# Kernel optimization log

Hardware: AMD Instinct MI355X
Metric: run time of the kernel (lower is better)

## Reference

```python
import jax, jax.numpy as jnp
import numpy as np
import math

N_EMBD = 768
N_HEAD = 12
D_HEAD = N_EMBD // N_HEAD  # 64, used ONLY for the score scale (matches the torch code)
B, S = 4, 2048


def setup_inputs() -> dict:
    key = jax.random.key(0)
    ks = jax.random.split(key, 9)
    scale = 1.0 / math.sqrt(N_EMBD)
    return {
        "x": jax.random.normal(ks[0], (B, S, N_EMBD), dtype=jnp.float32),
        # per-head full-width projections, stacked over heads: [H, E, E]
        "Wq": jax.random.normal(ks[1], (N_HEAD, N_EMBD, N_EMBD), dtype=jnp.float32) * scale,
        "Wk": jax.random.normal(ks[2], (N_HEAD, N_EMBD, N_EMBD), dtype=jnp.float32) * scale,
        "Wv": jax.random.normal(ks[3], (N_HEAD, N_EMBD, N_EMBD), dtype=jnp.float32) * scale,
        "bq": jax.random.normal(ks[4], (N_HEAD, N_EMBD), dtype=jnp.float32) * scale,
        "bk": jax.random.normal(ks[5], (N_HEAD, N_EMBD), dtype=jnp.float32) * scale,
        "bv": jax.random.normal(ks[6], (N_HEAD, N_EMBD), dtype=jnp.float32) * scale,
        # output projection: [H*E, E]
        "W0": jax.random.normal(ks[7], (N_HEAD * N_EMBD, N_EMBD), dtype=jnp.float32) * (1.0 / math.sqrt(N_HEAD * N_EMBD)),
        "b0": jax.random.normal(ks[8], (N_EMBD,), dtype=jnp.float32) * scale,
    }


def reference(x, Wq, Wk, Wv, bq, bk, bv, W0, b0):
    # Per-head projections, vectorized over heads: [B, H, S, E]
    q = jnp.einsum("bse,hef->bhsf", x, Wq) + bq[None, :, None, :]
    k = jnp.einsum("bse,hef->bhsf", x, Wk) + bk[None, :, None, :]
    v = jnp.einsum("bse,hef->bhsf", x, Wv) + bv[None, :, None, :]
    # scores: q @ k^T / sqrt(d_head)  (note: scale uses d_head, NOT n_embd, per source)
    scores = jnp.einsum("bhse,bhte->bhst", q, k) / math.sqrt(D_HEAD)
    attn = jax.nn.softmax(scores, axis=-1)  # no causal mask in the source
    y = jnp.einsum("bhst,bhte->bhse", attn, v)  # [B, H, S, E]
    # concat heads along feature dim in head order: [B, S, H*E]
    z = jnp.transpose(y, (0, 2, 1, 3)).reshape(B, S, N_HEAD * N_EMBD)
    return z @ W0 + b0
```

## Files before the change

### kernel.cpp

```cpp
#include <hip/hip_runtime.h>
#include <cstdint>
#include <cstddef>


#define DEV __device__ __forceinline__

using bf16x8 = __attribute__((ext_vector_type(8))) short;
using f32x4  = __attribute__((ext_vector_type(4))) float;
using su8    = __attribute__((ext_vector_type(8))) unsigned short;

DEV unsigned short f2b(float x) {
  unsigned u = __builtin_bit_cast(unsigned, x);
  u += 0x7fffu + ((u >> 16) & 1u);
  return (unsigned short)(u >> 16);
}

DEV void gld_lds16(const void* g, void* l) {
  __builtin_amdgcn_global_load_lds(
      (const __attribute__((address_space(1))) void*)g,
      (__attribute__((address_space(3))) void*)l,
      16, 0, 0);
}

template <int EPI>
__global__ __launch_bounds__(256)
void gemm_bt_k(const unsigned short* __restrict__ A, long az, int lda,
               const unsigned short* __restrict__ Bt, long bz, int ldb,
               void* __restrict__ C, long cz, int ldc,
               int K, float scale, const float* __restrict__ bias, int biasz)
{
  __shared__ unsigned short lsA[128 * 32];
  __shared__ unsigned short lsB[128 * 32];

  const int tid  = threadIdx.x;
  const int lane = tid & 63;
  const int wid  = tid >> 6;
  const int wr   = wid >> 1, wc = wid & 1;
  const int z    = blockIdx.z;
  const int m0   = blockIdx.x * 128;
  const int n0   = blockIdx.y * 128;

  A  += (size_t)z * az;
  Bt += (size_t)z * bz;

  f32x4 acc[4][4];
#pragma unroll
  for (int i = 0; i < 4; i++)
#pragma unroll
    for (int j = 0; j < 4; j++) acc[i][j] = (f32x4){0.f, 0.f, 0.f, 0.f};

  const int srow = lane >> 2;
  const int scol = (lane & 3) * 8;
  const int fr   = lane & 15;
  const int kq   = lane >> 4;

  for (int k0 = 0; k0 < K; k0 += 32) {
    __syncthreads();
#pragma unroll
    for (int i = 0; i < 2; i++) {
      int c = wid * 2 + i;
      int r = c * 16 + srow;
      gld_lds16(A  + (size_t)(m0 + r) * lda + (k0 + scol), &lsA[c * 512]);
      gld_lds16(Bt + (size_t)(n0 + r) * ldb + (k0 + scol), &lsB[c * 512]);
    }
    __syncthreads();

    bf16x8 af[4], bfr[4];
#pragma unroll
    for (int mi = 0; mi < 4; mi++)
      af[mi] = *(const bf16x8*)&lsA[(wr * 64 + mi * 16 + fr) * 32 + kq * 8];
#pragma unroll
    for (int ni = 0; ni < 4; ni++)
      bfr[ni] = *(const bf16x8*)&lsB[(wc * 64 + ni * 16 + fr) * 32 + kq * 8];
#pragma unroll
    for (int mi = 0; mi < 4; mi++)
#pragma unroll
      for (int ni = 0; ni < 4; ni++)
        acc[mi][ni] = __builtin_amdgcn_mfma_f32_16x16x32_bf16(af[mi], bfr[ni], acc[mi][ni], 0, 0, 0);
  }

  const int rb = m0 + wr * 64 + (lane >> 4) * 4;
  const int cb = n0 + wc * 64 + (lane & 15);

  if (EPI == 0) {
    unsigned short* Co = (unsigned short*)C + (size_t)z * cz;
#pragma unroll
    for (int mi = 0; mi < 4; mi++)
#pragma unroll
      for (int ni = 0; ni < 4; ni++) {
        int col = cb + ni * 16;
        float badd = bias ? bias[(size_t)z * biasz + col] : 0.f;
#pragma unroll
        for (int r = 0; r < 4; r++) {
          float v = acc[mi][ni][r] * scale + badd;
          Co[(size_t)(rb + mi * 16 + r) * ldc + col] = f2b(v);
        }
      }
  } else if (EPI == 1) {
    float* Co = (float*)C + (size_t)z * cz;
#pragma unroll
    for (int mi = 0; mi < 4; mi++)
#pragma unroll
      for (int ni = 0; ni < 4; ni++) {
        int col = cb + ni * 16;
#pragma unroll
        for (int r = 0; r < 4; r++)
          atomicAdd(&Co[(size_t)(rb + mi * 16 + r) * ldc + col], acc[mi][ni][r]);
      }
  } else {
    float* Co = (float*)C + (size_t)z * cz;
#pragma unroll
    for (int mi = 0; mi < 4; mi++)
#pragma unroll
      for (int ni = 0; ni < 4; ni++) {
        int col = cb + ni * 16;
#pragma unroll
        for (int r = 0; r < 4; r++)
          Co[(size_t)(rb + mi * 16 + r) * ldc + col] = acc[mi][ni][r] * scale;
      }
  }
}

__global__ __launch_bounds__(256)
void cast_k(const float* __restrict__ s, unsigned short* __restrict__ d, long n4)
{
  long i = (long)blockIdx.x * 256 + threadIdx.x;
  long stride = (long)gridDim.x * 256;
  for (; i < n4; i += stride) {
    float4 v = ((const float4*)s)[i];
    ushort4 o = { f2b(v.x), f2b(v.y), f2b(v.z), f2b(v.w) };
    ((ushort4*)d)[i] = o;
  }
}

__global__ __launch_bounds__(256)
void tcast_k(const float* __restrict__ src, unsigned short* __restrict__ dst)
{
  __shared__ unsigned short t[64][65];
  const int R = 768;
  const int r0 = blockIdx.x * 64, c0 = blockIdx.y * 64;
  const float* s = src + (size_t)blockIdx.z * R * R;
  unsigned short* d = dst + (size_t)blockIdx.z * R * R;
  const int tx = threadIdx.x & 63, ty = threadIdx.x >> 6;
#pragma unroll
  for (int i = 0; i < 16; i++) {
    int r = ty * 16 + i;
    t[r][tx] = f2b(s[(size_t)(r0 + r) * R + c0 + tx]);
  }
  __syncthreads();
#pragma unroll
  for (int i = 0; i < 16; i++) {
    int r = ty * 16 + i;
    d[(size_t)(c0 + r) * R + r0 + tx] = t[tx][r];
  }
}

__global__ __launch_bounds__(256)
void obias1_k(const float* __restrict__ pbv, const float* __restrict__ pW0,
              float* __restrict__ obp)
{
  int f = blockIdx.x * 256 + threadIdx.x;
  int c = blockIdx.y;
  int g0 = c * 256;
  float a = 0.f;
#pragma unroll 4
  for (int g = g0; g < g0 + 256; ++g) a += pbv[g] * pW0[(size_t)g * 768 + f];
  obp[(size_t)c * 768 + f] = a;
}

__global__ __launch_bounds__(256)
void obias2_k(const float* __restrict__ pb0, const float* __restrict__ obp,
              float* __restrict__ ob)
{
  int f = blockIdx.x * 256 + threadIdx.x;
  float a = pb0[f];
#pragma unroll
  for (int c = 0; c < 36; ++c) a += obp[(size_t)c * 768 + f];
  ob[f] = a;
}

__global__ __launch_bounds__(256)
void init_out_k(float4* __restrict__ out, const float4* __restrict__ ob, long n4)
{
  long i = (long)blockIdx.x * 256 + threadIdx.x;
  long stride = (long)gridDim.x * 256;
  for (; i < n4; i += stride) out[i] = ob[i % 192];
}

__global__ __launch_bounds__(256)
void softmax_rows_k(float* __restrict__ Sb)
{
  const int t = threadIdx.x;
  float* rowf = Sb + ((size_t)blockIdx.y * 2048 + blockIdx.x) * 2048;
  float4 a = ((const float4*)rowf)[t * 2];
  float4 b = ((const float4*)rowf)[t * 2 + 1];
  float v[8] = {a.x, a.y, a.z, a.w, b.x, b.y, b.z, b.w};

  float m = v[0];
#pragma unroll
  for (int j = 1; j < 8; j++) m = fmaxf(m, v[j]);
#pragma unroll
  for (int o = 1; o < 64; o <<= 1) m = fmaxf(m, __shfl_xor(m, o));
  __shared__ float red[8];
  if ((t & 63) == 0) red[t >> 6] = m;
  __syncthreads();
  m = fmaxf(fmaxf(red[0], red[1]), fmaxf(red[2], red[3]));

  float e[8], s = 0.f;
#pragma unroll
  for (int j = 0; j < 8; j++) { e[j] = __expf(v[j] - m); s += e[j]; }
#pragma unroll
  for (int o = 1; o < 64; o <<= 1) s += __shfl_xor(s, o);
  if ((t & 63) == 0) red[4 + (t >> 6)] = s;
  __syncthreads();
  s = red[4] + red[5] + red[6] + red[7];
  float rs = 1.f / s;

  unsigned short* rowb = (unsigned short*)rowf;
  su8 o8;
#pragma unroll
  for (int j = 0; j < 8; j++) o8[j] = f2b(e[j] * rs);
  *(su8*)&rowb[t * 8] = o8;
}

extern "C" void kernel_launch(void* const* d_in, const int* in_sizes, int n_in,
                              void* d_out, int out_size, void* d_ws, size_t ws_size,
                              hipStream_t stream)
{
  const long E = 768, S = 2048, H = 12, NB = 4;
  const long EE = E * E;
  const long SE = S * E;
  const long SS = S * S;

  const float* x   = (const float*)d_in[0];
  const float* Wq  = (const float*)d_in[1];
  const float* Wk  = (const float*)d_in[2];
  const float* Wv  = (const float*)d_in[3];
  const float* bq  = (const float*)d_in[4];
  const float* bk  = (const float*)d_in[5];
  const float* bv  = (const float*)d_in[6];
  const float* W0  = (const float*)d_in[7];
  const float* pb0 = (const float*)d_in[8];
  float* out = (float*)d_out;

  char* w = (char*)d_ws;
  size_t off = 0;
  auto take = [&](size_t bytes) -> char* {
    char* p = w + off;
    off += (bytes + 255) & ~(size_t)255;
    return p;
  };
  unsigned short* xb    = (unsigned short*)take(NB * SE * 2);
  unsigned short* WqTb  = (unsigned short*)take(H * EE * 2);
  unsigned short* WkTb  = (unsigned short*)take(H * EE * 2);
  unsigned short* WvpT  = (unsigned short*)take(H * EE * 2);
  unsigned short* Qb    = (unsigned short*)take(H * SE * 2);
  unsigned short* Kb    = (unsigned short*)take(H * SE * 2);
  unsigned short* VpT   = (unsigned short*)take(H * SE * 2);
  float*          obp   = (float*)take(36 * 768 * 4);
  float*          ob    = (float*)take(768 * 4);
  unsigned short* Wvb   = Qb;
  unsigned short* W0Tb  = Kb;

  size_t rem = (ws_size > off) ? (ws_size - off) : 0;
  int G = 1;
  if      ((size_t)12 * SS * 4 <= rem) G = 12;
  else if ((size_t)4  * SS * 4 <= rem) G = 4;
  else if ((size_t)2  * SS * 4 <= rem) G = 2;
  float* Sb = (float*)take((size_t)G * SS * 4);

  cast_k<<<2048, 256, 0, stream>>>(x,  xb,  NB * SE / 4);
  cast_k<<<2048, 256, 0, stream>>>(Wv, Wvb, H * EE / 4);
  tcast_k<<<dim3(12, 12, 12), 256, 0, stream>>>(Wq, WqTb);
  tcast_k<<<dim3(12, 12, 12), 256, 0, stream>>>(Wk, WkTb);
  tcast_k<<<dim3(12, 12, 12), 256, 0, stream>>>(W0, W0Tb);

  gemm_bt_k<0><<<dim3(6, 6, 12), 256, 0, stream>>>(
      W0Tb, EE, 768, Wvb, EE, 768, WvpT, EE, 768, 768, 1.f, nullptr, 0);

  obias1_k<<<dim3(3, 36), 256, 0, stream>>>(bv, W0, obp);
  obias2_k<<<3, 256, 0, stream>>>(pb0, obp, ob);
  init_out_k<<<2048, 256, 0, stream>>>((float4*)out, (const float4*)ob, NB * SE / 4);

  for (int b = 0; b < 4; b++) {
    const unsigned short* xbB = xb + (size_t)b * SE;

    gemm_bt_k<0><<<dim3(16, 6, 12), 256, 0, stream>>>(
        xbB, 0, 768, WqTb, EE, 768, Qb, SE, 768, 768, 1.f, bq, 768);
    gemm_bt_k<0><<<dim3(16, 6, 12), 256, 0, stream>>>(
        xbB, 0, 768, WkTb, EE, 768, Kb, SE, 768, 768, 1.f, bk, 768);
    gemm_bt_k<0><<<dim3(6, 16, 12), 256, 0, stream>>>(
        WvpT, EE, 768, xbB, 0, 768, VpT, SE, 2048, 768, 1.f, nullptr, 0);

    for (int g = 0; g < 12; g += G) {
      gemm_bt_k<2><<<dim3(16, 16, G), 256, 0, stream>>>(
          Qb + (size_t)g * SE, SE, 768, Kb + (size_t)g * SE, SE, 768,
          Sb, SS, 2048, 768, 0.125f, nullptr, 0);
      softmax_rows_k<<<dim3(2048, G), 256, 0, stream>>>(Sb);
      gemm_bt_k<1><<<dim3(16, 6, G), 256, 0, stream>>>(
          (const unsigned short*)Sb, SS * 2, 4096, VpT + (size_t)g * SE, SE, 2048,
          out + (size_t)b * SE, 0, 768, 2048, 1.f, nullptr, 0);
    }
  }
}
```

Baseline: 2.432 ms.

## Fold Q/K projections into per-head Wq·Wk^T and use 256x256 pipelined GEMM

Replaces the 128x128 GEMM kernel with a 512-thread 256x256 tile kernel that uses double-buffered, XOR-swizzled LDS, staged global-to-LDS loads, split MFMA phases and setprio. It also rewrites the attention algebra: it precomputes M = Wq·Wk^T per head and T = x·M, so scores are T·x^T plus a per-key bias x·(Wk·bq). This removes the separate Q and K projections; the q·bk terms are softmax-invariant and dropped. The trade-off is a large tile that needs 128KB of LDS per block, plus extra precompute kernels.

```diff
diff --git a/kernel.cpp b/kernel.cpp
--- a/kernel.cpp
+++ b/kernel.cpp
@@ -22,101 +22,194 @@
       16, 0, 0);
 }
 
+#define BAR() __builtin_amdgcn_s_barrier()
+#define VMCNT4() asm volatile("s_waitcnt vmcnt(4)" ::: "memory")
+
+DEV void stage_half(const unsigned short* __restrict__ g, int ldx, int grow0,
+                    int k0, char* region, int h, int wid, int lane) {
+  const int rbase = h * 128 + wid * 16;
+  const int colb = ((lane & 7) * 16) ^ ((lane >> 3) << 4);
+#pragma unroll
+  for (int j = 0; j < 2; ++j) {
+    char* dst = region + (rbase + j * 8) * 128;
+    const char* src = (const char*)(g + (size_t)(grow0 + rbase + j * 8 + (lane >> 3)) * ldx + k0) + colb;
+    gld_lds16(src, dst);
+  }
+}
+
+DEV bf16x8 ldread(const char* region, int r, int kel) {
+  int lin = r * 128 + kel * 2;
+  lin ^= (r & 7) << 4;
+  return *(const bf16x8*)(region + lin);
+}
+
 template <int EPI>
-__global__ __launch_bounds__(256)
-void gemm_bt_k(const unsigned short* __restrict__ A, long az, int lda,
-               const unsigned short* __restrict__ Bt, long bz, int ldb,
-               void* __restrict__ C, long cz, int ldc,
-               int K, float scale, const float* __restrict__ bias, int biasz)
-{
-  __shared__ unsigned short lsA[128 * 32];
-  __shared__ unsigned short lsB[128 * 32];
-
+__global__ __launch_bounds__(512, 1)
+void gemm8_k(const unsigned short* __restrict__ A, long az, int lda,
+             const unsigned short* __restrict__ Bt, long bz, int ldb,
+             void* __restrict__ C, long cz, int ldc,
+             int K, float scale, const float* __restrict__ bias, long biasz)
+{
+  extern __shared__ char smem[];
   const int tid  = threadIdx.x;
   const int lane = tid & 63;
   const int wid  = tid >> 6;
-  const int wr   = wid >> 1, wc = wid & 1;
+  const int wr   = wid >> 2;
+  const int wcn  = wid & 3;
   const int z    = blockIdx.z;
-  const int m0   = blockIdx.x * 128;
-  const int n0   = blockIdx.y * 128;
-
+  const int m0   = blockIdx.x * 256;
+  const int n0   = blockIdx.y * 256;
   A  += (size_t)z * az;
   Bt += (size_t)z * bz;
-
-  f32x4 acc[4][4];
-#pragma unroll
-  for (int i = 0; i < 4; i++)
-#pragma unroll
-    for (int j = 0; j < 4; j++) acc[i][j] = (f32x4){0.f, 0.f, 0.f, 0.f};
-
-  const int srow = lane >> 2;
-  const int scol = (lane & 3) * 8;
-  const int fr   = lane & 15;
-  const int kq   = lane >> 4;
-
-  for (int k0 = 0; k0 < K; k0 += 32) {
-    __syncthreads();
-#pragma unroll
-    for (int i = 0; i < 2; i++) {
-      int c = wid * 2 + i;
-      int r = c * 16 + srow;
-      gld_lds16(A  + (size_t)(m0 + r) * lda + (k0 + scol), &lsA[c * 512]);
-      gld_lds16(Bt + (size_t)(n0 + r) * ldb + (k0 + scol), &lsB[c * 512]);
-    }
-    __syncthreads();
-
-    bf16x8 af[4], bfr[4];
-#pragma unroll
-    for (int mi = 0; mi < 4; mi++)
-      af[mi] = *(const bf16x8*)&lsA[(wr * 64 + mi * 16 + fr) * 32 + kq * 8];
-#pragma unroll
-    for (int ni = 0; ni < 4; ni++)
-      bfr[ni] = *(const bf16x8*)&lsB[(wc * 64 + ni * 16 + fr) * 32 + kq * 8];
-#pragma unroll
-    for (int mi = 0; mi < 4; mi++)
-#pragma unroll
-      for (int ni = 0; ni < 4; ni++)
-        acc[mi][ni] = __builtin_amdgcn_mfma_f32_16x16x32_bf16(af[mi], bfr[ni], acc[mi][ni], 0, 0, 0);
-  }
-
-  const int rb = m0 + wr * 64 + (lane >> 4) * 4;
-  const int cb = n0 + wc * 64 + (lane & 15);
-
+  const int NT = K >> 6;
+
+  f32x4 acc[8][4];
+#pragma unroll
+  for (int i = 0; i < 8; ++i)
+#pragma unroll
+    for (int j = 0; j < 4; ++j) acc[i][j] = (f32x4){0.f, 0.f, 0.f, 0.f};
+
+  char* A0r = smem;
+  char* B0r = smem + 32768;
+  char* A1r = smem + 65536;
+  char* B1r = smem + 65536 + 32768;
+
+  stage_half(A,  lda, m0, 0, A0r, 0, wid, lane);
+  stage_half(A,  lda, m0, 0, A0r, 1, wid, lane);
+  stage_half(Bt, ldb, n0, 0, B0r, 0, wid, lane);
+  stage_half(Bt, ldb, n0, 0, B0r, 1, wid, lane);
+  if (NT > 1) {
+    stage_half(A, lda, m0, 64, A1r, 0, wid, lane);
+    stage_half(A, lda, m0, 64, A1r, 1, wid, lane);
+    VMCNT4();
+  } else {
+    asm volatile("s_waitcnt vmcnt(0)" ::: "memory");
+  }
+  BAR();
+
+  const int fr = lane & 15;
+  const int kq = (lane >> 4) * 8;
+
+  for (int t = 0; t < NT; ++t) {
+    const int s = t & 1;
+    const char* Ar = smem + s * 65536;
+    const char* Br = Ar + 32768;
+    char* Bn = smem + (s ^ 1) * 65536 + 32768;
+    char* An = smem + s * 65536;
+    const int kB = (t + 1) * 64, kA = (t + 2) * 64;
+
+    bf16x8 aLo[4][2], aHi[4][2], bLo[2][2], bHi[2][2];
+
+    if (t + 1 < NT) stage_half(Bt, ldb, n0, kB, Bn, 0, wid, lane);
+#pragma unroll
+    for (int m = 0; m < 4; ++m)
+#pragma unroll
+      for (int ks = 0; ks < 2; ++ks)
+        aLo[m][ks] = ldread(Ar, wr * 128 + m * 16 + fr, ks * 32 + kq);
+#pragma unroll
+    for (int n = 0; n < 2; ++n)
+#pragma unroll
+      for (int ks = 0; ks < 2; ++ks)
+        bLo[n][ks] = ldread(Br, wcn * 64 + n * 16 + fr, ks * 32 + kq);
+    BAR();
+    __builtin_amdgcn_s_setprio(1);
+#pragma unroll
+    for (int m = 0; m < 4; ++m)
+#pragma unroll
+      for (int n = 0; n < 2; ++n)
+#pragma unroll
+        for (int ks = 0; ks < 2; ++ks)
+          acc[m][n] = __builtin_amdgcn_mfma_f32_16x16x32_bf16(aLo[m][ks], bLo[n][ks], acc[m][n], 0, 0, 0);
+    __builtin_amdgcn_s_setprio(0);
+    BAR();
+
+    if (t + 1 < NT) stage_half(Bt, ldb, n0, kB, Bn, 1, wid, lane);
+#pragma unroll
+    for (int m = 0; m < 4; ++m)
+#pragma unroll
+      for (int ks = 0; ks < 2; ++ks)
+        aHi[m][ks] = ldread(Ar, wr * 128 + 64 + m * 16 + fr, ks * 32 + kq);
+    BAR();
+    __builtin_amdgcn_s_setprio(1);
+#pragma unroll
+    for (int m = 0; m < 4; ++m)
+#pragma unroll
+      for (int n = 0; n < 2; ++n)
+#pragma unroll
+        for (int ks = 0; ks < 2; ++ks)
+          acc[4 + m][n] = __builtin_amdgcn_mfma_f32_16x16x32_bf16(aHi[m][ks], bLo[n][ks], acc[4 + m][n], 0, 0, 0);
+    __builtin_amdgcn_s_setprio(0);
+    BAR();
+
+    if (t + 2 < NT) stage_half(A, lda, m0, kA, An, 0, wid, lane);
+#pragma unroll
+    for (int n = 0; n < 2; ++n)
+#pragma unroll
+      for (int ks = 0; ks < 2; ++ks)
+        bHi[n][ks] = ldread(Br, wcn * 64 + 32 + n * 16 + fr, ks * 32 + kq);
+    BAR();
+    __builtin_amdgcn_s_setprio(1);
+#pragma unroll
+    for (int m = 0; m < 4; ++m)
+#pragma unroll
+      for (int n = 0; n < 2; ++n)
+#pragma unroll
+        for (int ks = 0; ks < 2; ++ks)
+          acc[m][2 + n] = __builtin_amdgcn_mfma_f32_16x16x32_bf16(aLo[m][ks], bHi[n][ks], acc[m][2 + n], 0, 0, 0);
+    __builtin_amdgcn_s_setprio(0);
+    BAR();
+
+    if (t + 2 < NT) stage_half(A, lda, m0, kA, An, 1, wid, lane);
+    BAR();
+    __builtin_amdgcn_s_setprio(1);
+#pragma unroll
+    for (int m = 0; m < 4; ++m)
+#pragma unroll
+      for (int n = 0; n < 2; ++n)
+#pragma unroll
+        for (int ks = 0; ks < 2; ++ks)
+          acc[4 + m][2 + n] = __builtin_amdgcn_mfma_f32_16x16x32_bf16(aHi[m][ks], bHi[n][ks], acc[4 + m][2 + n], 0, 0, 0);
+    __builtin_amdgcn_s_setprio(0);
+    VMCNT4();
+    BAR();
+  }
+
+  const int rb = m0 + wr * 128 + (lane >> 4) * 4;
+  const int cb = n0 + wcn * 64 + fr;
   if (EPI == 0) {
     unsigned short* Co = (unsigned short*)C + (size_t)z * cz;
 #pragma unroll
-    for (int mi = 0; mi < 4; mi++)
-#pragma unroll
-      for (int ni = 0; ni < 4; ni++) {
-        int col = cb + ni * 16;
-        float badd = bias ? bias[(size_t)z * biasz + col] : 0.f;
-#pragma unroll
-        for (int r = 0; r < 4; r++) {
-          float v = acc[mi][ni][r] * scale + badd;
-          Co[(size_t)(rb + mi * 16 + r) * ldc + col] = f2b(v);
-        }
+    for (int mi = 0; mi < 8; ++mi)
+#pragma unroll
+      for (int ni = 0; ni < 4; ++ni) {
+        const int col = cb + ni * 16;
+        const float badd = bias ? bias[(size_t)z * biasz + col] : 0.f;
+#pragma unroll
+        for (int r = 0; r < 4; ++r)
+          Co[(size_t)(rb + mi * 16 + r) * ldc + col] = f2b(acc[mi][ni][r] * scale + badd);
       }
   } else if (EPI == 1) {
     float* Co = (float*)C + (size_t)z * cz;
 #pragma unroll
-    for (int mi = 0; mi < 4; mi++)
-#pragma unroll
-      for (int ni = 0; ni < 4; ni++) {
-        int col = cb + ni * 16;
-#pragma unroll
-        for (int r = 0; r < 4; r++)
-          atomicAdd(&Co[(size_t)(rb + mi * 16 + r) * ldc + col], acc[mi][ni][r]);
+    for (int mi = 0; mi < 8; ++mi)
+#pragma unroll
+      for (int ni = 0; ni < 4; ++ni) {
+        const int col = cb + ni * 16;
+#pragma unroll
+        for (int r = 0; r < 4; ++r)
+          atomicAdd(&Co[(size_t)(rb + mi * 16 + r) * ldc + col], acc[mi][ni][r] * scale);
       }
   } else {
     float* Co = (float*)C + (size_t)z * cz;
 #pragma unroll
-    for (int mi = 0; mi < 4; mi++)
-#pragma unroll
-      for (int ni = 0; ni < 4; ni++) {
-        int col = cb + ni * 16;
-#pragma unroll
-        for (int r = 0; r < 4; r++)
-          Co[(size_t)(rb + mi * 16 + r) * ldc + col] = acc[mi][ni][r] * scale;
+    for (int mi = 0; mi < 8; ++mi)
+#pragma unroll
+      for (int ni = 0; ni < 4; ++ni) {
+        const int col = cb + ni * 16;
+        const float badd = bias ? bias[(size_t)z * biasz + col] : 0.f;
+#pragma unroll
+        for (int r = 0; r < 4; ++r)
+          Co[(size_t)(rb + mi * 16 + r) * ldc + col] = (acc[mi][ni][r] + badd) * scale;
       }
   }
 }
@@ -152,6 +245,45 @@
   for (int i = 0; i < 16; i++) {
     int r = ty * 16 + i;
     d[(size_t)(c0 + r) * R + r0 + tx] = t[tx][r];
+  }
+}
+
+__global__ __launch_bounds__(256)
+void wv2_k(const float* __restrict__ Wk, const float* __restrict__ bq,
+           float* __restrict__ wv2)
+{
+  int gw = blockIdx.x * 4 + (threadIdx.x >> 6);
+  int lane = threadIdx.x & 63;
+  int h = gw / 768, e = gw % 768;
+  const float* wrow = Wk + ((size_t)h * 768 + e) * 768;
+  const float* b = bq + (size_t)h * 768;
+  float a = 0.f;
+#pragma unroll
+  for (int j = 0; j < 12; ++j) a += wrow[lane + j * 64] * b[lane + j * 64];
+#pragma unroll
+  for (int o = 1; o < 64; o <<= 1) a += __shfl_xor(a, o);
+  if (!lane) wv2[gw] = a;
+}
+
+__global__ __launch_bounds__(256)
+void vbias_k(const float* __restrict__ x, const float* __restrict__ wv2,
+             float* __restrict__ vb)
+{
+  int gw = blockIdx.x * 4 + (threadIdx.x >> 6);
+  int lane = threadIdx.x & 63;
+  int b = gw >> 11, t = gw & 2047;
+  const float* xr = x + ((size_t)b * 2048 + t) * 768;
+  float xv[12];
+#pragma unroll
+  for (int j = 0; j < 12; ++j) xv[j] = xr[lane + j * 64];
+#pragma unroll
+  for (int h = 0; h < 12; ++h) {
+    float a = 0.f;
+#pragma unroll
+    for (int j = 0; j < 12; ++j) a += xv[j] * wv2[(size_t)h * 768 + lane + j * 64];
+#pragma unroll
+    for (int o = 1; o < 64; o <<= 1) a += __shfl_xor(a, o);
+    if (!lane) vb[((size_t)b * 12 + h) * 2048 + t] = a;
   }
 }
 
@@ -231,13 +363,13 @@
   const long EE = E * E;
   const long SE = S * E;
   const long SS = S * S;
+  const size_t LDSB = 131072;
 
   const float* x   = (const float*)d_in[0];
   const float* Wq  = (const float*)d_in[1];
   const float* Wk  = (const float*)d_in[2];
   const float* Wv  = (const float*)d_in[3];
   const float* bq  = (const float*)d_in[4];
-  const float* bk  = (const float*)d_in[5];
   const float* bv  = (const float*)d_in[6];
   const float* W0  = (const float*)d_in[7];
   const float* pb0 = (const float*)d_in[8];
@@ -250,32 +382,40 @@
     off += (bytes + 255) & ~(size_t)255;
     return p;
   };
-  unsigned short* xb    = (unsigned short*)take(NB * SE * 2);
-  unsigned short* WqTb  = (unsigned short*)take(H * EE * 2);
-  unsigned short* WkTb  = (unsigned short*)take(H * EE * 2);
-  unsigned short* WvpT  = (unsigned short*)take(H * EE * 2);
-  unsigned short* Qb    = (unsigned short*)take(H * SE * 2);
-  unsigned short* Kb    = (unsigned short*)take(H * SE * 2);
-  unsigned short* VpT   = (unsigned short*)take(H * SE * 2);
-  float*          obp   = (float*)take(36 * 768 * 4);
-  float*          ob    = (float*)take(768 * 4);
-  unsigned short* Wvb   = Qb;
-  unsigned short* W0Tb  = Kb;
+  unsigned short* xb   = (unsigned short*)take(NB * SE * 2);
+  unsigned short* Mtb  = (unsigned short*)take(H * EE * 2);
+  unsigned short* WvpT = (unsigned short*)take(H * EE * 2);
+  unsigned short* Tb   = (unsigned short*)take(H * SE * 2);
+  unsigned short* VpT  = (unsigned short*)take(H * SE * 2);
+  float* wv2 = (float*)take(H * E * 4);
+  float* vb  = (float*)take(NB * H * S * 4);
+  float* obp = (float*)take(36 * 768 * 4);
+  float* ob  = (float*)take(768 * 4);
+  unsigned short* Wqb  = Tb;
+  unsigned short* Wkb  = Tb + H * EE;
+  unsigned short* Wvb  = VpT;
+  unsigned short* W0Tb = VpT + H * EE;
 
   size_t rem = (ws_size > off) ? (ws_size - off) : 0;
   int G = 1;
   if      ((size_t)12 * SS * 4 <= rem) G = 12;
+  else if ((size_t)6  * SS * 4 <= rem) G = 6;
   else if ((size_t)4  * SS * 4 <= rem) G = 4;
+  else if ((size_t)3  * SS * 4 <= rem) G = 3;
   else if ((size_t)2  * SS * 4 <= rem) G = 2;
   float* Sb = (float*)take((size_t)G * SS * 4);
 
   cast_k<<<2048, 256, 0, stream>>>(x,  xb,  NB * SE / 4);
+  cast_k<<<2048, 256, 0, stream>>>(Wq, Wqb, H * EE / 4);
+  cast_k<<<2048, 256, 0, stream>>>(Wk, Wkb, H * EE / 4);
   cast_k<<<2048, 256, 0, stream>>>(Wv, Wvb, H * EE / 4);
-  tcast_k<<<dim3(12, 12, 12), 256, 0, stream>>>(Wq, WqTb);
-  tcast_k<<<dim3(12, 12, 12), 256, 0, stream>>>(Wk, WkTb);
   tcast_k<<<dim3(12, 12, 12), 256, 0, stream>>>(W0, W0Tb);
-
-  gemm_bt_k<0><<<dim3(6, 6, 12), 256, 0, stream>>>(
+  wv2_k<<<H * 768 / 4, 256, 0, stream>>>(Wk, bq, wv2);
+  vbias_k<<<NB * 2048 / 4, 256, 0, stream>>>(x, wv2, vb);
+
+  gemm8_k<0><<<dim3(3, 3, 12), 512, LDSB, stream>>>(
+      Wkb, EE, 768, Wqb, EE, 768, Mtb, EE, 768, 768, 1.f, nullptr, 0);
+  gemm8_k<0><<<dim3(3, 3, 12), 512, LDSB, stream>>>(
       W0Tb, EE, 768, Wvb, EE, 768, WvpT, EE, 768, 768, 1.f, nullptr, 0);
 
   obias1_k<<<dim3(3, 36), 256, 0, stream>>>(bv, W0, obp);
@@ -285,19 +425,17 @@
   for (int b = 0; b < 4; b++) {
     const unsigned short* xbB = xb + (size_t)b * SE;
 
-    gemm_bt_k<0><<<dim3(16, 6, 12), 256, 0, stream>>>(
-        xbB, 0, 768, WqTb, EE, 768, Qb, SE, 768, 768, 1.f, bq, 768);
-    gemm_bt_k<0><<<dim3(16, 6, 12), 256, 0, stream>>>(
-        xbB, 0, 768, WkTb, EE, 768, Kb, SE, 768, 768, 1.f, bk, 768);
-    gemm_bt_k<0><<<dim3(6, 16, 12), 256, 0, stream>>>(
+    gemm8_k<0><<<dim3(8, 3, 12), 512, LDSB, stream>>>(
+        xbB, 0, 768, Mtb, EE, 768, Tb, SE, 768, 768, 1.f, nullptr, 0);
+    gemm8_k<0><<<dim3(3, 8, 12), 512, LDSB, stream>>>(
         WvpT, EE, 768, xbB, 0, 768, VpT, SE, 2048, 768, 1.f, nullptr, 0);
 
     for (int g = 0; g < 12; g += G) {
-      gemm_bt_k<2><<<dim3(16, 16, G), 256, 0, stream>>>(
-          Qb + (size_t)g * SE, SE, 768, Kb + (size_t)g * SE, SE, 768,
-          Sb, SS, 2048, 768, 0.125f, nullptr, 0);
+      gemm8_k<2><<<dim3(8, 8, G), 512, LDSB, stream>>>(
+          Tb + (size_t)g * SE, SE, 768, xbB, 0, 768,
+          Sb, SS, 2048, 768, 0.125f, vb + ((size_t)b * 12 + g) * 2048, 2048);
       softmax_rows_k<<<dim3(2048, G), 256, 0, stream>>>(Sb);
-      gemm_bt_k<1><<<dim3(16, 6, G), 256, 0, stream>>>(
+      gemm8_k<1><<<dim3(8, 3, G), 512, LDSB, stream>>>(
           (const unsigned short*)Sb, SS * 2, 4096, VpT + (size_t)g * SE, SE, 2048,
           out + (size_t)b * SE, 0, 768, 2048, 1.f, nullptr, 0);
     }
```

New measurement: 2.010 ms. 1.21x faster.
